# Kernel tuning notes

Measured on AMD Instinct MI355X. Metric: run time of the kernel, lower is better.

The kernel has to match this reference:

```python
import jax, jax.numpy as jnp
import numpy as np
from jax import lax

ROUTINGS = 3
SCALING = 2
NUM_CAPSULE = 8
NUM_ATOMS = 16
EPS = 1e-9


def squash(v):
    # SegCaps squash: v * |v|^2 / ((1+|v|^2) * |v|), norm over last axis
    sq = jnp.sum(v * v, axis=-1, keepdims=True)
    return v * sq / ((1.0 + sq) * jnp.sqrt(sq + EPS))


def setup_inputs() -> dict:
    key = jax.random.key(0)
    k1, k2 = jax.random.split(key)
    B, H, Wd, Cin, Ain = 4, 56, 56, 8, 32
    x = jax.random.normal(k1, (B, H, Wd, Cin, Ain), dtype=jnp.float32)
    # TF conv2d_transpose filter layout: [k, k, out_ch, in_ch]
    W = jax.random.normal(k2, (4, 4, NUM_CAPSULE * NUM_ATOMS, Ain), dtype=jnp.float32) * 0.05
    b = 0.1 * jnp.ones((1, 1, NUM_CAPSULE, NUM_ATOMS), dtype=jnp.float32)
    return {"x": x, "W": W, "b": b}


def reference(x, W, b):
    B, H, Wd, Cin, Ain = x.shape
    Cout, Aout = NUM_CAPSULE, NUM_ATOMS
    # [B,H,W,Cin,A] -> [Cin,B,H,W,A] -> [Cin*B,H,W,A]  (faithful to original ordering)
    xt = jnp.transpose(x, (3, 0, 1, 2, 4)).reshape(Cin * B, H, Wd, Ain)
    # TF conv2d_transpose, SAME padding, stride=scaling: out spatial = in * scaling
    out = lax.conv_transpose(
        xt, W, strides=(SCALING, SCALING), padding="SAME",
        dimension_numbers=("NHWC", "HWIO", "NHWC"), transpose_kernel=True)
    Hp, Wp = out.shape[1], out.shape[2]
    # votes: [B, Cin, Hp, Wp, Cout, Aout]  (faithful to original reshape)
    votes = out.reshape(B, Cin, Hp, Wp, Cout, Aout)
    biases = jnp.broadcast_to(b, (Hp, Wp, Cout, Aout))
    logits = jnp.zeros((B, Cin, Hp, Wp, Cout), dtype=x.dtype)
    act = None
    for i in range(ROUTINGS):
        route = jax.nn.softmax(logits, axis=-1)                      # [B,Cin,Hp,Wp,Cout]
        pre = jnp.einsum("bihwc,bihwca->bhwca", route, votes) + biases
        act = squash(pre)                                            # [B,Hp,Wp,Cout,Aout]
        if i < ROUTINGS - 1:
            logits = logits + jnp.einsum("bihwca,bhwca->bihwc", votes, act)
    return act
```

## Files before the change

### kernel.cpp

```cpp
#include <hip/hip_runtime.h>
#include <math.h>

#define CEPS 1e-9f

typedef _Float16 half8 __attribute__((ext_vector_type(8)));
typedef _Float16 h2 __attribute__((ext_vector_type(2)));
typedef __fp16 fp16x2 __attribute__((ext_vector_type(2)));
typedef float floatx16 __attribute__((ext_vector_type(16)));


template<int CTRL>
__device__ __forceinline__ float dpp_add(float v) {
    return v + __int_as_float(__builtin_amdgcn_update_dpp(
        0, __float_as_int(v), CTRL, 0xF, 0xF, false));
}
__device__ __forceinline__ h2 pkrtz(float a, float b) {
    return __builtin_bit_cast(h2, __builtin_amdgcn_cvt_pkrtz(a, b));
}
__device__ __forceinline__ float fdot2(h2 a, h2 b, float c) {
    return __builtin_amdgcn_fdot2(__builtin_bit_cast(fp16x2, a),
                                  __builtin_bit_cast(fp16x2, b), c, false);
}

__global__ __launch_bounds__(256, 5) void caps_mfma(
    const float* __restrict__ x,
    const float* __restrict__ Wt,
    const float* __restrict__ bias,
    float* __restrict__ out)
{
    __shared__ __align__(16) unsigned char smem[32768];
    _Float16* xt   = (_Float16*)smem;
    _Float16* wt16 = (_Float16*)(smem + 16384);
    _Float16* scx  = (_Float16*)smem;

    const int tid = threadIdx.x;
    const int tile = blockIdx.x;
    const int tu = tile / 14, tv = tile - tu * 14;
    const int u0 = tu * 4, v0 = tv * 4;
    const int rh = blockIdx.y >> 1;
    const int rw = blockIdx.y & 1;
    const int bp = blockIdx.z;

    #pragma unroll
    for (int it = 0; it < 4; ++it) {
        int idx = tid + (it << 8);
        if (idx < 800) {
            int cell = idx >> 5;
            int r = idx & 31;
            int i = r >> 2;
            int ci0 = (r & 3) << 3;
            int ri = cell / 5, rj = cell - ri * 5;
            int gi = u0 + rh - 1 + ri;
            int gj = v0 + rw - 1 + rj;
            float tmp[8] = {0.f, 0.f, 0.f, 0.f, 0.f, 0.f, 0.f, 0.f};
            if ((unsigned)gi < 56u && (unsigned)gj < 56u) {
                const float* src = x + (((i & 3) * 56 + gi) * 56 + gj) * 256
                                     + ((bp * 2 + (i >> 2)) << 5) + ci0;
                float4 a0 = *(const float4*)src;
                float4 a1 = *(const float4*)(src + 4);
                tmp[0] = a0.x; tmp[1] = a0.y; tmp[2] = a0.z; tmp[3] = a0.w;
                tmp[4] = a1.x; tmp[5] = a1.y; tmp[6] = a1.z; tmp[7] = a1.w;
            }
            half8 hv;
            #pragma unroll
            for (int j = 0; j < 8; ++j) hv[j] = (_Float16)tmp[j];
            *(half8*)(xt + (cell * 8 + i) * 40 + ci0) = hv;
        }
    }

    #pragma unroll
    for (int k = 0; k < 4; ++k) {
        int en = tid + (k << 8);
        int s  = en >> 7;
        int t  = (en >> 6) & 1;
        int ll = en & 63;
        int n  = t * 32 + (ll & 31);
        int hh = ll >> 5;
        int ci0 = ((s & 1) << 4) + (hh << 3);
        int kh = ((s >> 2) << 1) + 1 - rh;
        int kw = (((s >> 1) & 1) << 1) + 1 - rw;
        const float* src = Wt + (((kh * 4 + kw) * 128 + n) << 5) + ci0;
        float4 w0 = *(const float4*)src;
        float4 w1 = *(const float4*)(src + 4);
        half8 hv;
        hv[0] = (_Float16)w0.x; hv[1] = (_Float16)w0.y;
        hv[2] = (_Float16)w0.z; hv[3] = (_Float16)w0.w;
        hv[4] = (_Float16)w1.x; hv[5] = (_Float16)w1.y;
        hv[6] = (_Float16)w1.z; hv[7] = (_Float16)w1.w;
        *(half8*)(wt16 + (en << 3)) = hv;
    }
    __syncthreads();

    const int l = tid & 63;
    const int w = tid >> 6;
    const int col = l & 31, h = l >> 5;
    const int invA = (l & 31) * 40 + (h << 3);

    const int e = l & 1;
    const int c = (l >> 1) & 7;
    const int pl = l >> 4;
    h2 bq[4];
    {
        const float* bpt = bias + (c << 4) + (e << 3);
        float4 b0 = *(const float4*)bpt;
        float4 b1 = *(const float4*)(bpt + 4);
        bq[0] = pkrtz(b0.x, b0.y); bq[1] = pkrtz(b0.z, b0.w);
        bq[2] = pkrtz(b1.x, b1.y); bq[3] = pkrtz(b1.z, b1.w);
    }

    h2 pf[4][8];
    #pragma unroll
    for (int hf = 0; hf < 2; ++hf) {
        floatx16 acc0, acc1;
        #pragma unroll
        for (int j = 0; j < 16; ++j) { acc0[j] = 0.f; acc1[j] = 0.f; }
        const int tb = hf << 1;
        #pragma unroll
        for (int s = 0; s < 8; ++s) {
            const int tkh = s >> 2;
            const int tkw = (s >> 1) & 1;
            const int row = w + 1 - tkh;
            int aoff = (row * 5 + 1 - tkw) * 320 + ((s & 1) << 4) + invA;
            asm("" : "+v"(aoff));
            half8 af = *(const half8*)(xt + aoff);

            int boff0 = ((((s << 1) + 0) * 64 + l) << 4);
            int boff1 = ((((s << 1) + 1) * 64 + l) << 4);
            asm volatile("" : "+v"(boff0));
            asm volatile("" : "+v"(boff1));
            half8 bf0 = *(const half8*)((const unsigned char*)wt16 + boff0);
            half8 bf1 = *(const half8*)((const unsigned char*)wt16 + boff1);

            acc0 = __builtin_amdgcn_mfma_f32_32x32x16_f16(af, bf0, acc0, 0, 0, 0);
            acc1 = __builtin_amdgcn_mfma_f32_32x32x16_f16(af, bf1, acc1, 0, 0, 0);
        }
        #pragma unroll
        for (int m = 0; m < 8; ++m) {
            pf[tb][m]     = pkrtz(acc0[2 * m], acc0[2 * m + 1]);
            pf[tb + 1][m] = pkrtz(acc1[2 * m], acc1[2 * m + 1]);
        }
        __builtin_amdgcn_sched_barrier(0);
        if (hf == 0) {
            __syncthreads();
            #pragma unroll
            for (int k = 0; k < 4; ++k) {
                int en = tid + (k << 8);
                int s  = en >> 7;
                int t  = (en >> 6) & 1;
                int ll = en & 63;
                int n  = (t + 2) * 32 + (ll & 31);
                int hh = ll >> 5;
                int ci0 = ((s & 1) << 4) + (hh << 3);
                int kh = ((s >> 2) << 1) + 1 - rh;
                int kw = (((s >> 1) & 1) << 1) + 1 - rw;
                const float* src = Wt + (((kh * 4 + kw) * 128 + n) << 5) + ci0;
                float4 w0 = *(const float4*)src;
                float4 w1 = *(const float4*)(src + 4);
                half8 hv;
                hv[0] = (_Float16)w0.x; hv[1] = (_Float16)w0.y;
                hv[2] = (_Float16)w0.z; hv[3] = (_Float16)w0.w;
                hv[4] = (_Float16)w1.x; hv[5] = (_Float16)w1.y;
                hv[6] = (_Float16)w1.z; hv[7] = (_Float16)w1.w;
                *(half8*)(wt16 + (en << 3)) = hv;
            }
            __syncthreads();
        }
    }

    __syncthreads();

    _Float16* wbW = scx + (w << 12);
    {
        _Float16* wp = wbW + (h << 9) + col;
        #pragma unroll
        for (int t = 0; t < 4; ++t)
            #pragma unroll
            for (int m = 0; m < 8; ++m) {
                h2 pp = pf[t][m];
                const int mpl = m >> 1;
                const int il0 = (2 * m) & 3;
                const int il1 = (2 * m + 1) & 3;
                wp[mpl * 1024 + il0 * 128 + t * 32] = pp[0];
                wp[mpl * 1024 + il1 * 128 + t * 32] = pp[1];
            }
    }

    h2 va[8][4];
    {
        const _Float16* rp = wbW + (pl << 10) + (c << 4) + (e << 3);
        #pragma unroll
        for (int i = 0; i < 8; ++i) {
            half8 vv = *(const half8*)(rp + (i << 7));
            va[i][0][0] = vv[0]; va[i][0][1] = vv[1];
            va[i][1][0] = vv[2]; va[i][1][1] = vv[3];
            va[i][2][0] = vv[4]; va[i][2][1] = vv[5];
            va[i][3][0] = vv[6]; va[i][3][1] = vv[7];
        }
    }

    const h2 c0125 = pkrtz(0.125f, 0.125f);
    h2 pre[4];
    float lgv[8];

    #pragma unroll
    for (int d = 0; d < 4; ++d) {
        h2 s01 = va[0][d] + va[1][d];
        h2 s23 = va[2][d] + va[3][d];
        h2 s45 = va[4][d] + va[5][d];
        h2 s67 = va[6][d] + va[7][d];
        h2 s = (s01 + s23) + (s45 + s67);
        pre[d] = s * c0125 + bq[d];
    }
    {
        float n = fdot2(pre[0], pre[0], 0.f);
        n = fdot2(pre[1], pre[1], n);
        n = fdot2(pre[2], pre[2], n);
        n = fdot2(pre[3], pre[3], n);
        float nq = dpp_add<0xB1>(n);
        float sc = nq * __builtin_amdgcn_rcpf(1.f + nq)
                      * __builtin_amdgcn_rsqf(nq + CEPS);
        h2 sc2 = pkrtz(sc, sc);
        #pragma unroll
        for (int d = 0; d < 4; ++d) pre[d] *= sc2;
    }
    #pragma unroll
    for (int i = 0; i < 8; ++i) {
        float p = fdot2(va[i][0], pre[0], 0.f);
        p = fdot2(va[i][1], pre[1], p);
        p = fdot2(va[i][2], pre[2], p);
        p = fdot2(va[i][3], pre[3], p);
        lgv[i] = dpp_add<0xB1>(p);
    }

    #pragma unroll
    for (int r = 1; r < 3; ++r) {
        h2 rt2[8];
        #pragma unroll
        for (int i = 0; i < 8; ++i) {
            float ee = __expf(lgv[i]);
            float ss = dpp_add<0x4E>(ee);
            ss = dpp_add<0x141>(ss);
            ss = dpp_add<0x128>(ss);
            float route = ee * __builtin_amdgcn_rcpf(ss);
            rt2[i] = pkrtz(route, route);
        }
        #pragma unroll
        for (int d = 0; d < 4; ++d) {
            h2 p0 = rt2[0] * va[0][d], p1 = rt2[1] * va[1][d];
            h2 p2 = rt2[2] * va[2][d], p3 = rt2[3] * va[3][d];
            h2 p4 = rt2[4] * va[4][d], p5 = rt2[5] * va[5][d];
            h2 p6 = rt2[6] * va[6][d], p7 = rt2[7] * va[7][d];
            h2 s = ((p0 + p1) + (p2 + p3)) + ((p4 + p5) + (p6 + p7));
            pre[d] = s + bq[d];
        }
        {
            float n = fdot2(pre[0], pre[0], 0.f);
            n = fdot2(pre[1], pre[1], n);
            n = fdot2(pre[2], pre[2], n);
            n = fdot2(pre[3], pre[3], n);
            float nq = dpp_add<0xB1>(n);
            float sc = nq * __builtin_amdgcn_rcpf(1.f + nq)
                          * __builtin_amdgcn_rsqf(nq + CEPS);
            h2 sc2 = pkrtz(sc, sc);
            #pragma unroll
            for (int d = 0; d < 4; ++d) pre[d] *= sc2;
        }
        if (r < 2) {
            #pragma unroll
            for (int i = 0; i < 8; ++i) {
                float p = fdot2(va[i][0], pre[0], 0.f);
                p = fdot2(va[i][1], pre[1], p);
                p = fdot2(va[i][2], pre[2], p);
                p = fdot2(va[i][3], pre[3], p);
                lgv[i] += dpp_add<0xB1>(p);
            }
        }
    }

    {
        const int p = ((u0 + w) << 1) + rh;
        const int q = ((v0 + pl) << 1) + rw;
        float* op = out + (((bp * 112 + p) * 112 + q) << 7) + (c << 4) + (e << 3);
        float4 o0 = make_float4((float)pre[0][0], (float)pre[0][1],
                                (float)pre[1][0], (float)pre[1][1]);
        float4 o1 = make_float4((float)pre[2][0], (float)pre[2][1],
                                (float)pre[3][0], (float)pre[3][1]);
        *(float4*)op = o0;
        *(float4*)(op + 4) = o1;
    }
}

extern "C" void kernel_launch(void* const* d_in, const int* in_sizes, int n_in,
                              void* d_out, int out_size, void* d_ws, size_t ws_size,
                              hipStream_t stream) {
    const float* x  = (const float*)d_in[0];
    const float* Wt = (const float*)d_in[1];
    const float* b  = (const float*)d_in[2];
    float* out = (float*)d_out;
    (void)d_ws; (void)ws_size;

    dim3 grid(196, 4, 4);
    caps_mfma<<<grid, 256, 0, stream>>>(x, Wt, b, out);
}
```

Before: 109.1 us.

## Double-buffer weight tiles in LDS and prefetch next tile during MFMA

Splits the weight staging area into two LDS regions, each holding one 32-column slice. The loop now runs over four column tiles with a single accumulator, and issues global loads for the next slice before the MFMA loop, writing them to LDS one step later. This hides global load latency behind compute instead of stalling on a synchronous reload halfway through. In exchange it adds more __syncthreads calls and extra live prefetch registers, and each A fragment is now reloaded once per tile rather than once per pair of tiles.

Result: slower. 112.9 us (+3.5%).

```diff
diff --git a/kernel.cpp b/kernel.cpp
--- a/kernel.cpp
+++ b/kernel.cpp
@@ -20,6 +20,14 @@
 __device__ __forceinline__ float fdot2(h2 a, h2 b, float c) {
     return __builtin_amdgcn_fdot2(__builtin_bit_cast(fp16x2, a),
                                   __builtin_bit_cast(fp16x2, b), c, false);
+}
+__device__ __forceinline__ half8 cvt8(float4 a, float4 b) {
+    half8 hv;
+    hv[0] = (_Float16)a.x; hv[1] = (_Float16)a.y;
+    hv[2] = (_Float16)a.z; hv[3] = (_Float16)a.w;
+    hv[4] = (_Float16)b.x; hv[5] = (_Float16)b.y;
+    hv[6] = (_Float16)b.z; hv[7] = (_Float16)b.w;
+    return hv;
 }
 
 __global__ __launch_bounds__(256, 5) void caps_mfma(
@@ -30,7 +38,8 @@
 {
     __shared__ __align__(16) unsigned char smem[32768];
     _Float16* xt   = (_Float16*)smem;
-    _Float16* wt16 = (_Float16*)(smem + 16384);
+    _Float16* regA = (_Float16*)(smem + 16384);
+    _Float16* regB = (_Float16*)(smem + 24576);
     _Float16* scx  = (_Float16*)smem;
 
     const int tid = threadIdx.x;
@@ -69,25 +78,23 @@
     }
 
     #pragma unroll
-    for (int k = 0; k < 4; ++k) {
-        int en = tid + (k << 8);
-        int s  = en >> 7;
-        int t  = (en >> 6) & 1;
-        int ll = en & 63;
-        int n  = t * 32 + (ll & 31);
-        int hh = ll >> 5;
-        int ci0 = ((s & 1) << 4) + (hh << 3);
-        int kh = ((s >> 2) << 1) + 1 - rh;
-        int kw = (((s >> 1) & 1) << 1) + 1 - rw;
-        const float* src = Wt + (((kh * 4 + kw) * 128 + n) << 5) + ci0;
-        float4 w0 = *(const float4*)src;
-        float4 w1 = *(const float4*)(src + 4);
-        half8 hv;
-        hv[0] = (_Float16)w0.x; hv[1] = (_Float16)w0.y;
-        hv[2] = (_Float16)w0.z; hv[3] = (_Float16)w0.w;
-        hv[4] = (_Float16)w1.x; hv[5] = (_Float16)w1.y;
-        hv[6] = (_Float16)w1.z; hv[7] = (_Float16)w1.w;
-        *(half8*)(wt16 + (en << 3)) = hv;
+    for (int rgi = 0; rgi < 2; ++rgi) {
+        _Float16* dst = rgi ? regB : regA;
+        #pragma unroll
+        for (int k = 0; k < 2; ++k) {
+            int en = tid + (k << 8);
+            int s  = en >> 6;
+            int ll = en & 63;
+            int n  = rgi * 32 + (ll & 31);
+            int hh = ll >> 5;
+            int ci0 = ((s & 1) << 4) + (hh << 3);
+            int kh = ((s >> 2) << 1) + 1 - rh;
+            int kw = (((s >> 1) & 1) << 1) + 1 - rw;
+            const float* src = Wt + (((kh * 4 + kw) * 128 + n) << 5) + ci0;
+            float4 w0 = *(const float4*)src;
+            float4 w1 = *(const float4*)(src + 4);
+            *(half8*)(dst + (en << 3)) = cvt8(w0, w1);
+        }
     }
     __syncthreads();
 
@@ -109,62 +116,63 @@
     }
 
     h2 pf[4][8];
-    #pragma unroll
-    for (int hf = 0; hf < 2; ++hf) {
-        floatx16 acc0, acc1;
-        #pragma unroll
-        for (int j = 0; j < 16; ++j) { acc0[j] = 0.f; acc1[j] = 0.f; }
-        const int tb = hf << 1;
+    float4 wpre[4];
+    half8 wh[2];
+    #pragma unroll
+    for (int tt = 0; tt < 4; ++tt) {
+        _Float16* breg = (tt & 1) ? regB : regA;
+
+        if (tt == 1 || tt == 2) {
+            _Float16* dst = (tt == 1) ? regA : regB;
+            #pragma unroll
+            for (int k = 0; k < 2; ++k) {
+                int en = tid + (k << 8);
+                *(half8*)(dst + (en << 3)) = wh[k];
+            }
+        }
+        if (tt < 2) {
+            const int tn = tt + 2;
+            #pragma unroll
+            for (int k = 0; k < 2; ++k) {
+                int en = tid + (k << 8);
+                int s  = en >> 6;
+                int ll = en & 63;
+                int n  = tn * 32 + (ll & 31);
+                int hh = ll >> 5;
+                int ci0 = ((s & 1) << 4) + (hh << 3);
+                int kh = ((s >> 2) << 1) + 1 - rh;
+                int kw = (((s >> 1) & 1) << 1) + 1 - rw;
+                const float* src = Wt + (((kh * 4 + kw) * 128 + n) << 5) + ci0;
+                wpre[2 * k]     = *(const float4*)src;
+                wpre[2 * k + 1] = *(const float4*)(src + 4);
+            }
+        }
+
+        floatx16 acc;
+        #pragma unroll
+        for (int j = 0; j < 16; ++j) acc[j] = 0.f;
         #pragma unroll
         for (int s = 0; s < 8; ++s) {
             const int tkh = s >> 2;
             const int tkw = (s >> 1) & 1;
             const int row = w + 1 - tkh;
             int aoff = (row * 5 + 1 - tkw) * 320 + ((s & 1) << 4) + invA;
-            asm("" : "+v"(aoff));
+            asm("" : "+v"(aoff) : "v"(tt));
             half8 af = *(const half8*)(xt + aoff);
-
-            int boff0 = ((((s << 1) + 0) * 64 + l) << 4);
-            int boff1 = ((((s << 1) + 1) * 64 + l) << 4);
-            asm volatile("" : "+v"(boff0));
-            asm volatile("" : "+v"(boff1));
-            half8 bf0 = *(const half8*)((const unsigned char*)wt16 + boff0);
-            half8 bf1 = *(const half8*)((const unsigned char*)wt16 + boff1);
-
-            acc0 = __builtin_amdgcn_mfma_f32_32x32x16_f16(af, bf0, acc0, 0, 0, 0);
-            acc1 = __builtin_amdgcn_mfma_f32_32x32x16_f16(af, bf1, acc1, 0, 0, 0);
-        }
-        #pragma unroll
-        for (int m = 0; m < 8; ++m) {
-            pf[tb][m]     = pkrtz(acc0[2 * m], acc0[2 * m + 1]);
-            pf[tb + 1][m] = pkrtz(acc1[2 * m], acc1[2 * m + 1]);
+            int boff = (((s << 6) + l) << 4);
+            asm("" : "+v"(boff) : "v"(tt));
+            half8 bf = *(const half8*)((const unsigned char*)breg + boff);
+            acc = __builtin_amdgcn_mfma_f32_32x32x16_f16(af, bf, acc, 0, 0, 0);
+        }
+        #pragma unroll
+        for (int m = 0; m < 8; ++m)
+            pf[tt][m] = pkrtz(acc[2 * m], acc[2 * m + 1]);
+        if (tt < 2) {
+            wh[0] = cvt8(wpre[0], wpre[1]);
+            wh[1] = cvt8(wpre[2], wpre[3]);
         }
         __builtin_amdgcn_sched_barrier(0);
-        if (hf == 0) {
-            __syncthreads();
-            #pragma unroll
-            for (int k = 0; k < 4; ++k) {
-                int en = tid + (k << 8);
-                int s  = en >> 7;
-                int t  = (en >> 6) & 1;
-                int ll = en & 63;
-                int n  = (t + 2) * 32 + (ll & 31);
-                int hh = ll >> 5;
-                int ci0 = ((s & 1) << 4) + (hh << 3);
-                int kh = ((s >> 2) << 1) + 1 - rh;
-                int kw = (((s >> 1) & 1) << 1) + 1 - rw;
-                const float* src = Wt + (((kh * 4 + kw) * 128 + n) << 5) + ci0;
-                float4 w0 = *(const float4*)src;
-                float4 w1 = *(const float4*)(src + 4);
-                half8 hv;
-                hv[0] = (_Float16)w0.x; hv[1] = (_Float16)w0.y;
-                hv[2] = (_Float16)w0.z; hv[3] = (_Float16)w0.w;
-                hv[4] = (_Float16)w1.x; hv[5] = (_Float16)w1.y;
-                hv[6] = (_Float16)w1.z; hv[7] = (_Float16)w1.w;
-                *(half8*)(wt16 + (en << 3)) = hv;
-            }
-            __syncthreads();
-        }
+        if (tt < 3) __syncthreads();
     }
 
     __syncthreads();
```
